# Kernel tuning notes

Measured on AMD Instinct MI355X. Metric: run time of the kernel, lower is better.

Reference implementation:

```python
import jax, jax.numpy as jnp
import numpy as np

N_QUBITS = 12
N_LAYERS = 2
DIM = 2 ** N_QUBITS  # 4096
BATCH = 1024


def _apply_gate(state, gate, qubit):
    """Apply a batched 2x2 gate to `qubit`. state: (b, 2^n) c64, gate: (b,2,2) c64.
    Mirrors torch _apply_single_qubit_gate: swap qubit axis to front, bmm, swap back."""
    b = state.shape[0]
    s = state.reshape((b,) + (2,) * N_QUBITS)
    ax = N_QUBITS - qubit  # qubit 0 is the last (least-significant) axis
    s = jnp.swapaxes(s, 1, ax)
    s = s.reshape(b, 2, DIM // 2)
    s = jnp.einsum('bij,bjk->bik', gate, s)
    s = s.reshape((b, 2) + (2,) * (N_QUBITS - 1))
    s = jnp.swapaxes(s, 1, ax)
    return s.reshape(b, DIM)


def _ry_gate(angle):
    """RY(theta) = [[cos(t/2), -sin(t/2)], [sin(t/2), cos(t/2)]]; angle: (b,)."""
    c = jnp.cos(angle / 2)
    s = jnp.sin(angle / 2)
    g = jnp.stack([jnp.stack([c, -s], axis=-1),
                   jnp.stack([s, c], axis=-1)], axis=-2)
    return g.astype(jnp.complex64)


def _apply_cnot(state, control, target):
    """CNOT: flip target amplitudes on the control=1 subspace."""
    b = state.shape[0]
    s = state.reshape((b,) + (2,) * N_QUBITS)
    ca = N_QUBITS - control
    ta = N_QUBITS - target
    s = jnp.moveaxis(s, (ca, ta), (1, 2))
    # control=0 slice unchanged; control=1 slice: swap target 0<->1 (flip)
    s = jnp.concatenate([s[:, :1], jnp.flip(s[:, 1:2], axis=2)], axis=1)
    s = jnp.moveaxis(s, (1, 2), (ca, ta))
    return s.reshape(b, DIM)


def _make_signs():
    # Pauli-Z expectation per qubit = sum_s probs[s] * (1 - 2*bit_q(s)); qubit 0 = LSB
    idx = np.arange(DIM)
    bits = (idx[:, None] >> np.arange(N_QUBITS)[None, :]) & 1
    return jnp.asarray(1.0 - 2.0 * bits, dtype=jnp.float32)  # (DIM, n_qubits)

SIGNS = _make_signs()


def setup_inputs() -> dict:
    key = jax.random.key(0)
    kx, kt = jax.random.split(key)
    x = jax.random.normal(kx, (BATCH, N_QUBITS), dtype=jnp.float32)
    thetas = 0.1 * jax.random.normal(kt, (N_LAYERS, N_QUBITS), dtype=jnp.float32)
    return {"x": x, "thetas": thetas}


def reference(x, thetas):
    b = x.shape[0]
    # |0>^n initial state
    state = jnp.zeros((b, DIM), dtype=jnp.complex64).at[:, 0].set(1.0)
    # angle encoding: RY(x_q) on each qubit
    for q in range(N_QUBITS):
        state = _apply_gate(state, _ry_gate(x[:, q]), q)
    # variational layers: RY(theta) per qubit, then cyclic CNOT ring
    for layer in range(N_LAYERS):
        for q in range(N_QUBITS):
            ang = jnp.broadcast_to(thetas[layer, q], (b,))
            state = _apply_gate(state, _ry_gate(ang), q)
        for q in range(N_QUBITS):
            state = _apply_cnot(state, q, (q + 1) % N_QUBITS)
    # Pauli-Z expectations on all qubits: (b, n_qubits)
    probs = jnp.abs(state) ** 2
    return probs @ SIGNS
```

## Files before the change

### kernel.cpp

```cpp
#include <hip/hip_runtime.h>

#define NQ    12
#define BATCH 1024

typedef float v2 __attribute__((ext_vector_type(2)));
typedef float v4 __attribute__((ext_vector_type(4)));

template<int P>
__device__ __forceinline__ void ryp_t(v2 A[16], float t) {
#pragma unroll
    for (int m = 0; m < 16; ++m) {
        if ((m & (1 << P)) == 0) {
            const int j = m | (1 << P);
            const v2 Ai = A[m], Aj = A[j];
            A[m] = Ai - t * Aj;
            A[j] = Aj + t * Ai;
        }
    }
}

__device__ __forceinline__ void ry0_t(v2 A[16], float t) {
    const v2 tv = v2{-t, t};
#pragma unroll
    for (int m = 0; m < 16; ++m) {
        const v2 sw = v2{A[m].y, A[m].x};
        A[m] = A[m] + tv * sw;
    }
}

__device__ __forceinline__ float rdlane(float v, int lane) {
    return __uint_as_float(__builtin_amdgcn_readlane(__float_as_uint(v), lane));
}

template<int CTRL>
__device__ __forceinline__ float dppx(float v) {
    return __int_as_float(__builtin_amdgcn_mov_dpp(__float_as_int(v), CTRL, 0xF, 0xF, true));
}
template<int PAT>
__device__ __forceinline__ float swz(float v) {
    return __int_as_float(__builtin_amdgcn_ds_swizzle(__float_as_int(v), PAT));
}

__global__ __launch_bounds__(512, 2)
void qc_kernel(const float* __restrict__ x, const float* __restrict__ th,
               float* __restrict__ out) {
    __shared__ __attribute__((aligned(16))) float buf1[4 * 4352];
    __shared__ float obuf[4 * 24];

    const int tid = threadIdx.x;
    const int p = tid >> 7;
    const int w = (tid >> 6) & 1;
    const int l = tid & 63;
    const int b = blockIdx.x * 4 + p;
    const float* xb = x + b * NQ;
    float* bufp  = &buf1[p * 4352];
    float* obufp = &obuf[p * 24];

    const int q_ = l & 31;
    float ang;
    if (l & 32) ang = (q_ < 12) ? 0.5f * th[NQ + q_] : 0.0f;
    else        { const int m_ = (q_ < 12) ? q_ : 11; ang = 0.5f * (xb[m_] + th[m_]); }
    float sv_, cv_;
    __sincosf(ang, &sv_, &cv_);
    const float tl = __fdividef(sv_, cv_);

    float pt = cv_;
    pt *= dppx<0xB1>(pt);
    pt *= dppx<0x4E>(pt);
    pt *= swz<0x101F>(pt);
    pt *= swz<0x201F>(pt);
    const float C = rdlane(pt, 32);

    float c_[NQ], s_[NQ], t1[NQ];
#pragma unroll
    for (int q = 0; q < NQ; ++q) {
        c_[q] = rdlane(cv_, q);
        s_[q] = rdlane(sv_, q);
        t1[q] = rdlane(tl, 32 + q);
    }

    const int l0=l&1, l1=(l>>1)&1, l2=(l>>2)&1, l3=(l>>3)&1, l4=(l>>4)&1, l5=(l>>5)&1;
    float GL = ((l1^l0) ? s_[6] : c_[6]) * ((l2^l1) ? s_[7] : c_[7]);
    GL *= ((l3^l2) ? s_[8] : c_[8]) * ((l4^l3) ? s_[9] : c_[9]);
    GL *= ((l5^l4) ? s_[10] : c_[10]) * ((w^l5) ? s_[11] : c_[11]);
    GL *= C;
    const float GL0 = GL * (l0 ? s_[5] : c_[5]);
    const float GL1 = GL * (l0 ? c_[5] : s_[5]);

    const float f0_0 = w ? s_[0] : c_[0], f0_1 = w ? c_[0] : s_[0];
    const float f1_0 = w ? s_[1] : c_[1], f1_1 = w ? c_[1] : s_[1];

    v2 A[16];
    A[0] = v2{f0_0 * f1_0, f0_1 * f1_1};
    A[1] = v2{f0_0 * f1_1, f0_1 * f1_0};
#pragma unroll
    for (int k = 2; k < 5; ++k) {
#pragma unroll
        for (int m = 0; m < (1 << (k - 1)); ++m) {
            const int bp = (m >> (k - 2)) & 1;
            A[m | (1 << (k - 1))] = A[m] * (bp ? c_[k] : s_[k]);
            A[m]                  = A[m] * (bp ? s_[k] : c_[k]);
        }
    }
#pragma unroll
    for (int m = 0; m < 16; ++m) A[m] *= (m & 8) ? GL1 : GL0;

    ry0_t(A, t1[0]);
    ryp_t<0>(A, t1[1]);
    ryp_t<1>(A, t1[2]);
    ryp_t<2>(A, t1[3]);
    ryp_t<3>(A, t1[4]);

    {
        float* wp = &bufp[w * 2176 + l];
#pragma unroll
        for (int m = 0; m < 16; ++m) {
            wp[(2*m)   * 68] = A[m].x;
            wp[(2*m+1) * 68] = A[m].y;
        }
    }
    __syncthreads();

    {
        const float s10 = (l & 32) ? t1[10] : -t1[10];
        const float s11 = w ? t1[11] : -t1[11];
        const int basec = (l & 31) * 68;
        const int ro = (l & 32);
        const int rf = ro ^ 32;
        const float* p00 = &bufp[ w      * 2176 + basec + ro];
        const float* p01 = &bufp[ w      * 2176 + basec + rf];
        const float* p10 = &bufp[(w ^ 1) * 2176 + basec + ro];
        const float* p11 = &bufp[(w ^ 1) * 2176 + basec + rf];
#pragma unroll
        for (int k = 0; k < 8; ++k) {
            const v4 a  = *reinterpret_cast<const v4*>(p00 + 4*k);
            const v4 bq = *reinterpret_cast<const v4*>(p01 + 4*k);
            const v4 cq = *reinterpret_cast<const v4*>(p10 + 4*k);
            const v4 dq = *reinterpret_cast<const v4*>(p11 + 4*k);
            const v4 u = a  + s10 * bq;
            const v4 v = cq + s10 * dq;
            const v4 r = u + s11 * v;
            A[2*k]   = v2{r.x, r.y};
            A[2*k+1] = v2{r.z, r.w};
        }
    }

    ry0_t(A, t1[5]);
    ryp_t<0>(A, t1[6]);
    ryp_t<1>(A, t1[7]);
    ryp_t<2>(A, t1[8]);
    ryp_t<3>(A, t1[9]);

#pragma unroll
    for (int m = 0; m < 16; ++m) A[m] *= A[m];

    v2 e[8], f[8];
#pragma unroll
    for (int i = 0; i < 8; ++i) { e[i] = A[2*i] + A[2*i+1]; f[i] = A[2*i] - A[2*i+1]; }
    v2 se = ((e[0]+e[1]) + (e[2]+e[3])) + ((e[4]+e[5]) + (e[6]+e[7]));
    v2 sf = ((f[0]+f[1]) + (f[2]+f[3])) + ((f[4]+f[5]) + (f[6]+f[7]));
    v2 gq[4];
#pragma unroll
    for (int j = 0; j < 4; ++j) gq[j] = f[2*j] - f[2*j+1];
    const v2 sg2 = (gq[0]+gq[1]) + (gq[2]+gq[3]);
    const v2 h0 = gq[0] - gq[1], h1 = gq[2] - gq[3];
    const v2 sh = h0 + h1;
    const v2 iv = h0 - h1;
    const float S  = se.x + se.y;
    const float P1 = se.x - se.y;
    const float P3 = sf.x - sf.y;
    const float P7 = sg2.x - sg2.y;
    const float PF = sh.x - sh.y;
    const float PV = iv.x - iv.y;

    const int pl5 = __popc(l & 31) & 1;
    float y0 = pl5 ? -P1 : P1;
    float y1 = pl5 ? -P3 : P3;
    float y2 = pl5 ? -P7 : P7;
    float y3 = pl5 ? -PF : PF;
    y0 += dppx<0xB1>(y0); y1 += dppx<0xB1>(y1);
    y2 += dppx<0xB1>(y2); y3 += dppx<0xB1>(y3);
    y0 += dppx<0x4E>(y0); y1 += dppx<0x4E>(y1);
    y2 += dppx<0x4E>(y2); y3 += dppx<0x4E>(y3);
    const int g = l & 3;
    float y = (g == 0) ? y0 : (g == 1) ? y1 : (g == 2) ? y2 : y3;
    y += swz<0x101F>(y);
    y += swz<0x201F>(y);
    y += swz<0x401F>(y);
    y += __shfl_xor(y, 32, 64);
    if (l < 4) obufp[(5 + l) * 2 + w] = y;

    const float sg0 = (l & 1)  ? -1.f : 1.f;
    const float sg1 = (l & 2)  ? -1.f : 1.f;
    const float sg2s = (l & 4) ? -1.f : 1.f;
    const float sg3 = (l & 8)  ? -1.f : 1.f;
    const float sg4 = (l & 16) ? -1.f : 1.f;
    const float sg5 = (l & 32) ? -1.f : 1.f;
    float wS = S, wV = PV;
    { const float pS = dppx<0xB1>(wS),  pV = dppx<0xB1>(wV);  wS = __builtin_fmaf(sg0, wS, pS); wV = __builtin_fmaf(sg0, wV, pV); }
    { const float pS = dppx<0x4E>(wS),  pV = dppx<0x4E>(wV);  wS = __builtin_fmaf(sg1, wS, pS); wV = __builtin_fmaf(sg1, wV, pV); }
    { const float pS = swz<0x101F>(wS), pV = swz<0x101F>(wV); wS = __builtin_fmaf(sg2s, wS, pS); wV = __builtin_fmaf(sg2s, wV, pV); }
    { const float pS = swz<0x201F>(wS), pV = swz<0x201F>(wV); wS = __builtin_fmaf(sg3, wS, pS); wV = __builtin_fmaf(sg3, wV, pV); }
    { const float pS = swz<0x401F>(wS), pV = swz<0x401F>(wV); wS = __builtin_fmaf(sg4, wS, pS); wV = __builtin_fmaf(sg4, wV, pV); }
    { const float pS = __shfl_xor(wS, 32, 64), pV = __shfl_xor(wV, 32, 64);
      wS = __builtin_fmaf(sg5, wS, pS); wV = __builtin_fmaf(sg5, wV, pV); }

    if (l == 3)  obufp[1*2 + w]  = wS;
    if (l == 7)  obufp[2*2 + w]  = wS;
    if (l == 15) obufp[3*2 + w]  = wS;
    if (l == 31) { obufp[4*2 + w] = wS; obufp[9*2 + w] = wV; }
    if (l == 62) obufp[0*2 + w]  = wV;
    if (l == 63) { obufp[10*2 + w] = wV; obufp[11*2 + w] = wV; }
    __syncthreads();

    if ((tid & 127) < NQ) {
        const int q = tid & 127;
        const float p0 = obufp[q*2 + 0], p1 = obufp[q*2 + 1];
        out[b * NQ + q] = (q == 0 || q == 11) ? (p0 - p1) : (p0 + p1);
    }
}

extern "C" void kernel_launch(void* const* d_in, const int* in_sizes, int n_in,
                              void* d_out, int out_size, void* d_ws, size_t ws_size,
                              hipStream_t stream) {
    const float* x  = (const float*)d_in[0];
    const float* th = (const float*)d_in[1];
    float* out = (float*)d_out;
    (void)in_sizes; (void)n_in; (void)out_size; (void)d_ws; (void)ws_size;

    qc_kernel<<<BATCH / 4, 512, 0, stream>>>(x, th, out);
}
```

Measured before the change: 9.682 us.

## Use one wavefront per batch element with 32 amplitudes per lane

Measured after the change: 9.723 us. About the same (+0.4%).

```diff
diff --git a/kernel.cpp b/kernel.cpp
--- a/kernel.cpp
+++ b/kernel.cpp
@@ -7,9 +7,9 @@
 typedef float v4 __attribute__((ext_vector_type(4)));
 
 template<int P>
-__device__ __forceinline__ void ryp_t(v2 A[16], float t) {
-#pragma unroll
-    for (int m = 0; m < 16; ++m) {
+__device__ __forceinline__ void ryp32_t(v2 A[32], float t) {
+#pragma unroll
+    for (int m = 0; m < 32; ++m) {
         if ((m & (1 << P)) == 0) {
             const int j = m | (1 << P);
             const v2 Ai = A[m], Aj = A[j];
@@ -19,10 +19,10 @@
     }
 }
 
-__device__ __forceinline__ void ry0_t(v2 A[16], float t) {
+__device__ __forceinline__ void ry032_t(v2 A[32], float t) {
     const v2 tv = v2{-t, t};
 #pragma unroll
-    for (int m = 0; m < 16; ++m) {
+    for (int m = 0; m < 32; ++m) {
         const v2 sw = v2{A[m].y, A[m].x};
         A[m] = A[m] + tv * sw;
     }
@@ -41,20 +41,14 @@
     return __int_as_float(__builtin_amdgcn_ds_swizzle(__float_as_int(v), PAT));
 }
 
-__global__ __launch_bounds__(512, 2)
+__global__ __launch_bounds__(64)
 void qc_kernel(const float* __restrict__ x, const float* __restrict__ th,
                float* __restrict__ out) {
-    __shared__ __attribute__((aligned(16))) float buf1[4 * 4352];
-    __shared__ float obuf[4 * 24];
-
-    const int tid = threadIdx.x;
-    const int p = tid >> 7;
-    const int w = (tid >> 6) & 1;
-    const int l = tid & 63;
-    const int b = blockIdx.x * 4 + p;
+    __shared__ __attribute__((aligned(16))) float buf[64 * 68];
+
+    const int b = blockIdx.x;
+    const int l = threadIdx.x;
     const float* xb = x + b * NQ;
-    float* bufp  = &buf1[p * 4352];
-    float* obufp = &obuf[p * 24];
 
     const int q_ = l & 31;
     float ang;
@@ -80,17 +74,16 @@
     }
 
     const int l0=l&1, l1=(l>>1)&1, l2=(l>>2)&1, l3=(l>>3)&1, l4=(l>>4)&1, l5=(l>>5)&1;
-    float GL = ((l1^l0) ? s_[6] : c_[6]) * ((l2^l1) ? s_[7] : c_[7]);
-    GL *= ((l3^l2) ? s_[8] : c_[8]) * ((l4^l3) ? s_[9] : c_[9]);
-    GL *= ((l5^l4) ? s_[10] : c_[10]) * ((w^l5) ? s_[11] : c_[11]);
-    GL *= C;
-    const float GL0 = GL * (l0 ? s_[5] : c_[5]);
-    const float GL1 = GL * (l0 ? c_[5] : s_[5]);
-
-    const float f0_0 = w ? s_[0] : c_[0], f0_1 = w ? c_[0] : s_[0];
-    const float f1_0 = w ? s_[1] : c_[1], f1_1 = w ? c_[1] : s_[1];
-
-    v2 A[16];
+    float GL = ((l1^l0) ? s_[7] : c_[7]) * ((l2^l1) ? s_[8] : c_[8]);
+    GL *= ((l3^l2) ? s_[9] : c_[9]) * ((l4^l3) ? s_[10] : c_[10]);
+    GL *= ((l5^l4) ? s_[11] : c_[11]) * C;
+    const float GL0 = GL * (l0 ? s_[6] : c_[6]);
+    const float GL1 = GL * (l0 ? c_[6] : s_[6]);
+
+    const float f0_0 = l5 ? s_[0] : c_[0], f0_1 = l5 ? c_[0] : s_[0];
+    const float f1_0 = l5 ? s_[1] : c_[1], f1_1 = l5 ? c_[1] : s_[1];
+
+    v2 A[32];
     A[0] = v2{f0_0 * f1_0, f0_1 * f1_1};
     A[1] = v2{f0_0 * f1_1, f0_1 * f1_0};
 #pragma unroll
@@ -102,19 +95,28 @@
             A[m]                  = A[m] * (bp ? s_[k] : c_[k]);
         }
     }
-#pragma unroll
-    for (int m = 0; m < 16; ++m) A[m] *= (m & 8) ? GL1 : GL0;
-
-    ry0_t(A, t1[0]);
-    ryp_t<0>(A, t1[1]);
-    ryp_t<1>(A, t1[2]);
-    ryp_t<2>(A, t1[3]);
-    ryp_t<3>(A, t1[4]);
-
     {
-        float* wp = &bufp[w * 2176 + l];
+        const float cH = c_[5] * GL1, sH = s_[5] * GL1;
+        const float cL = c_[5] * GL0, sL = s_[5] * GL0;
 #pragma unroll
         for (int m = 0; m < 16; ++m) {
+            const int bp = (m >> 3) & 1;
+            A[m | 16] = A[m] * (bp ? cH : sH);
+            A[m]      = A[m] * (bp ? sL : cL);
+        }
+    }
+
+    ry032_t(A, t1[0]);
+    ryp32_t<0>(A, t1[1]);
+    ryp32_t<1>(A, t1[2]);
+    ryp32_t<2>(A, t1[3]);
+    ryp32_t<3>(A, t1[4]);
+    ryp32_t<4>(A, t1[5]);
+
+    {
+        float* wp = &buf[l];
+#pragma unroll
+        for (int m = 0; m < 32; ++m) {
             wp[(2*m)   * 68] = A[m].x;
             wp[(2*m+1) * 68] = A[m].y;
         }
@@ -122,62 +124,55 @@
     __syncthreads();
 
     {
-        const float s10 = (l & 32) ? t1[10] : -t1[10];
-        const float s11 = w ? t1[11] : -t1[11];
-        const int basec = (l & 31) * 68;
-        const int ro = (l & 32);
-        const int rf = ro ^ 32;
-        const float* p00 = &bufp[ w      * 2176 + basec + ro];
-        const float* p01 = &bufp[ w      * 2176 + basec + rf];
-        const float* p10 = &bufp[(w ^ 1) * 2176 + basec + ro];
-        const float* p11 = &bufp[(w ^ 1) * 2176 + basec + rf];
-#pragma unroll
-        for (int k = 0; k < 8; ++k) {
-            const v4 a  = *reinterpret_cast<const v4*>(p00 + 4*k);
-            const v4 bq = *reinterpret_cast<const v4*>(p01 + 4*k);
-            const v4 cq = *reinterpret_cast<const v4*>(p10 + 4*k);
-            const v4 dq = *reinterpret_cast<const v4*>(p11 + 4*k);
-            const v4 u = a  + s10 * bq;
-            const v4 v = cq + s10 * dq;
-            const v4 r = u + s11 * v;
-            A[2*k]   = v2{r.x, r.y};
-            A[2*k+1] = v2{r.z, r.w};
-        }
-    }
-
-    ry0_t(A, t1[5]);
-    ryp_t<0>(A, t1[6]);
-    ryp_t<1>(A, t1[7]);
-    ryp_t<2>(A, t1[8]);
-    ryp_t<3>(A, t1[9]);
-
-#pragma unroll
-    for (int m = 0; m < 16; ++m) A[m] *= A[m];
-
-    v2 e[8], f[8];
-#pragma unroll
-    for (int i = 0; i < 8; ++i) { e[i] = A[2*i] + A[2*i+1]; f[i] = A[2*i] - A[2*i+1]; }
-    v2 se = ((e[0]+e[1]) + (e[2]+e[3])) + ((e[4]+e[5]) + (e[6]+e[7]));
-    v2 sf = ((f[0]+f[1]) + (f[2]+f[3])) + ((f[4]+f[5]) + (f[6]+f[7]));
-    v2 gq[4];
-#pragma unroll
-    for (int j = 0; j < 4; ++j) gq[j] = f[2*j] - f[2*j+1];
-    const v2 sg2 = (gq[0]+gq[1]) + (gq[2]+gq[3]);
-    const v2 h0 = gq[0] - gq[1], h1 = gq[2] - gq[3];
-    const v2 sh = h0 + h1;
-    const v2 iv = h0 - h1;
-    const float S  = se.x + se.y;
-    const float P1 = se.x - se.y;
-    const float P3 = sf.x - sf.y;
-    const float P7 = sg2.x - sg2.y;
-    const float PF = sh.x - sh.y;
-    const float PV = iv.x - iv.y;
-
-    const int pl5 = __popc(l & 31) & 1;
-    float y0 = pl5 ? -P1 : P1;
-    float y1 = pl5 ? -P3 : P3;
-    float y2 = pl5 ? -P7 : P7;
-    float y3 = pl5 ? -PF : PF;
+        const float* rp = &buf[l * 68];
+#pragma unroll
+        for (int k = 0; k < 16; ++k) {
+            const v4 t = *reinterpret_cast<const v4*>(rp + 4*k);
+            A[2*k]   = v2{t.x, t.y};
+            A[2*k+1] = v2{t.z, t.w};
+        }
+    }
+
+    ry032_t(A, t1[6]);
+    ryp32_t<0>(A, t1[7]);
+    ryp32_t<1>(A, t1[8]);
+    ryp32_t<2>(A, t1[9]);
+    ryp32_t<3>(A, t1[10]);
+    ryp32_t<4>(A, t1[11]);
+
+#pragma unroll
+    for (int m = 0; m < 32; ++m) A[m] *= A[m];
+
+    v2 e[16], f[16];
+#pragma unroll
+    for (int i = 0; i < 16; ++i) { e[i] = A[2*i] + A[2*i+1]; f[i] = A[2*i] - A[2*i+1]; }
+    const v2 se = (((e[0]+e[1])+(e[2]+e[3])) + ((e[4]+e[5])+(e[6]+e[7])))
+                + (((e[8]+e[9])+(e[10]+e[11])) + ((e[12]+e[13])+(e[14]+e[15])));
+    v2 fp[8], ff[8];
+#pragma unroll
+    for (int j = 0; j < 8; ++j) { fp[j] = f[2*j] + f[2*j+1]; ff[j] = f[2*j] - f[2*j+1]; }
+    const v2 sf1 = ((fp[0]+fp[1])+(fp[2]+fp[3])) + ((fp[4]+fp[5])+(fp[6]+fp[7]));
+    v2 fa[4], fff[4];
+#pragma unroll
+    for (int k = 0; k < 4; ++k) { fa[k] = ff[2*k] + ff[2*k+1]; fff[k] = ff[2*k] - ff[2*k+1]; }
+    const v2 sff  = (fa[0]+fa[1]) + (fa[2]+fa[3]);
+    const v2 sfff = (fff[0]+fff[1]) + (fff[2]+fff[3]);
+    const v2 g40 = fff[0] - fff[1], g41 = fff[2] - fff[3];
+    const v2 sg4 = g40 + g41;
+    const v2 g5  = g40 - g41;
+    const float S   = se.x + se.y;
+    const float P1  = se.x - se.y;
+    const float P3  = sf1.x - sf1.y;
+    const float P7  = sff.x - sff.y;
+    const float PF  = sfff.x - sfff.y;
+    const float PV5 = sg4.x - sg4.y;
+    const float PV6 = g5.x - g5.y;
+
+    const int pl = __popc(l) & 1;
+    float y0 = pl ? -P1 : P1;
+    float y1 = pl ? -P3 : P3;
+    float y2 = pl ? -P7 : P7;
+    float y3 = pl ? -PF : PF;
     y0 += dppx<0xB1>(y0); y1 += dppx<0xB1>(y1);
     y2 += dppx<0xB1>(y2); y3 += dppx<0xB1>(y3);
     y0 += dppx<0x4E>(y0); y1 += dppx<0x4E>(y1);
@@ -188,36 +183,36 @@
     y += swz<0x201F>(y);
     y += swz<0x401F>(y);
     y += __shfl_xor(y, 32, 64);
-    if (l < 4) obufp[(5 + l) * 2 + w] = y;
+
+    float y5 = pl ? -PV5 : PV5;
+    y5 += dppx<0xB1>(y5);
+    y5 += dppx<0x4E>(y5);
+    y5 += swz<0x101F>(y5);
+    y5 += swz<0x201F>(y5);
+    y5 += swz<0x401F>(y5);
+    y5 += __shfl_xor(y5, 32, 64);
 
     const float sg0 = (l & 1)  ? -1.f : 1.f;
     const float sg1 = (l & 2)  ? -1.f : 1.f;
-    const float sg2s = (l & 4) ? -1.f : 1.f;
+    const float sg2 = (l & 4)  ? -1.f : 1.f;
     const float sg3 = (l & 8)  ? -1.f : 1.f;
-    const float sg4 = (l & 16) ? -1.f : 1.f;
+    const float sg4s = (l & 16) ? -1.f : 1.f;
     const float sg5 = (l & 32) ? -1.f : 1.f;
-    float wS = S, wV = PV;
+    float wS = S, wV = PV6;
     { const float pS = dppx<0xB1>(wS),  pV = dppx<0xB1>(wV);  wS = __builtin_fmaf(sg0, wS, pS); wV = __builtin_fmaf(sg0, wV, pV); }
     { const float pS = dppx<0x4E>(wS),  pV = dppx<0x4E>(wV);  wS = __builtin_fmaf(sg1, wS, pS); wV = __builtin_fmaf(sg1, wV, pV); }
-    { const float pS = swz<0x101F>(wS), pV = swz<0x101F>(wV); wS = __builtin_fmaf(sg2s, wS, pS); wV = __builtin_fmaf(sg2s, wV, pV); }
+    { const float pS = swz<0x101F>(wS), pV = swz<0x101F>(wV); wS = __builtin_fmaf(sg2, wS, pS); wV = __builtin_fmaf(sg2, wV, pV); }
     { const float pS = swz<0x201F>(wS), pV = swz<0x201F>(wV); wS = __builtin_fmaf(sg3, wS, pS); wV = __builtin_fmaf(sg3, wV, pV); }
-    { const float pS = swz<0x401F>(wS), pV = swz<0x401F>(wV); wS = __builtin_fmaf(sg4, wS, pS); wV = __builtin_fmaf(sg4, wV, pV); }
+    { const float pS = swz<0x401F>(wS), pV = swz<0x401F>(wV); wS = __builtin_fmaf(sg4s, wS, pS); wV = __builtin_fmaf(sg4s, wV, pV); }
     { const float pS = __shfl_xor(wS, 32, 64), pV = __shfl_xor(wV, 32, 64);
       wS = __builtin_fmaf(sg5, wS, pS); wV = __builtin_fmaf(sg5, wV, pV); }
 
-    if (l == 3)  obufp[1*2 + w]  = wS;
-    if (l == 7)  obufp[2*2 + w]  = wS;
-    if (l == 15) obufp[3*2 + w]  = wS;
-    if (l == 31) { obufp[4*2 + w] = wS; obufp[9*2 + w] = wV; }
-    if (l == 62) obufp[0*2 + w]  = wV;
-    if (l == 63) { obufp[10*2 + w] = wV; obufp[11*2 + w] = wV; }
-    __syncthreads();
-
-    if ((tid & 127) < NQ) {
-        const int q = tid & 127;
-        const float p0 = obufp[q*2 + 0], p1 = obufp[q*2 + 1];
-        out[b * NQ + q] = (q == 0 || q == 11) ? (p0 - p1) : (p0 + p1);
-    }
+    float* ob = out + b * NQ;
+    if (l < 4)  ob[6 + l] = y;
+    if (l == 4) ob[10] = y5;
+    if (l >= 3 && ((l & (l + 1)) == 0)) ob[__popc(l) - 1] = wS;
+    if (l == 62) ob[0]  = wV;
+    if (l == 63) ob[11] = wV;
 }
 
 extern "C" void kernel_launch(void* const* d_in, const int* in_sizes, int n_in,
@@ -228,5 +223,5 @@
     float* out = (float*)d_out;
     (void)in_sizes; (void)n_in; (void)out_size; (void)d_ws; (void)ws_size;
 
-    qc_kernel<<<BATCH / 4, 512, 0, stream>>>(x, th, out);
-}
+    qc_kernel<<<BATCH, 64, 0, stream>>>(x, th, out);
+}
```
